# Optimization experiments

Measured on AMD Instinct MI355X. Metric: run time of the kernel, lower is better.

The kernel has to match this reference:

```python
import jax, jax.numpy as jnp
import numpy as np

N_POINTS = 131072
N_SEG = 16
C = 256
BN_EPS = 1e-5


def setup_inputs() -> dict:
    key = jax.random.key(0)
    ks = jax.random.split(key, 6)
    x = jax.random.normal(ks[0], (N_POINTS, C), jnp.float32)
    # Ragged segment end-offsets (cumulative counts), strictly increasing, last == N_POINTS.
    rng = np.random.default_rng(0)
    base = N_POINTS // N_SEG
    counts = base + rng.integers(-base // 32, base // 32, N_SEG)
    counts[-1] += N_POINTS - counts.sum()
    o = jnp.asarray(np.cumsum(counts), jnp.int32)
    s1 = 1.0 / np.sqrt(2 * C)  # linear1: Linear(2C -> C)
    s2 = 1.0 / np.sqrt(C)      # linear2: Linear(C -> C)
    W1 = jax.random.uniform(ks[1], (2 * C, C), jnp.float32, -s1, s1)
    b1 = jax.random.uniform(ks[2], (C,), jnp.float32, -s1, s1)
    W2 = jax.random.uniform(ks[3], (C, C), jnp.float32, -s2, s2)
    b2 = jax.random.uniform(ks[4], (C,), jnp.float32, -s2, s2)
    gamma = jnp.ones((C,), jnp.float32)
    beta = jnp.zeros((C,), jnp.float32)
    return {"x": x, "o": o, "W1": W1, "b1": b1, "W2": W2, "b2": b2,
            "gamma": gamma, "beta": beta}


def reference(x, o, W1, b1, W2, b2, gamma, beta):
    n, c = x.shape
    s = o.shape[0]
    # segment id per point from cumulative end-offsets
    seg_id = jnp.searchsorted(o, jnp.arange(n), side="right")  # [N]
    counts = jnp.concatenate([o[:1], o[1:] - o[:-1]])          # [S]
    # per-segment mean pooling (x_b.sum(0, True) / cnt)
    sums = jax.ops.segment_sum(x, seg_id, num_segments=s)      # [S, C]
    means = sums / counts[:, None].astype(x.dtype)
    # linear2: Linear(C, C) + ReLU on segment means
    y = jax.nn.relu(means @ W2 + b2)                           # [S, C]
    # broadcast-concat back to points, then linear1: Linear(2C, C)
    h = jnp.concatenate([x, y[seg_id]], axis=1) @ W1 + b1      # [N, C]
    # BatchNorm1d (training mode: batch statistics, biased variance) + ReLU
    mu = h.mean(axis=0)
    var = h.var(axis=0)
    out = jax.nn.relu((h - mu) * (gamma / jnp.sqrt(var + BN_EPS)) + beta)
    return out
```

## Files before the change

kernel.cpp:

```cpp
#include <hip/hip_runtime.h>
#include <stdint.h>

#define N_PTS 131072
#define NC 256
#define NSEG 16
#define BN_EPSF 1e-5f

typedef __attribute__((ext_vector_type(8))) short bf16x8;
typedef __attribute__((ext_vector_type(4))) float f32x4;

__device__ __forceinline__ unsigned short f2bf(float f) {
  union { float f; uint32_t u; } v; v.f = f;
  uint32_t u = v.u;
  uint32_t r = (u + 0x7fffu + ((u >> 16) & 1u)) >> 16;
  return (unsigned short)r;
}

__device__ __forceinline__ int swz(int col, int row) {
  return (col & ~63) | ((((col >> 3) & 7) ^ (row & 7)) << 3) | (col & 7);
}

__device__ __forceinline__ void gll16(const unsigned short* g, unsigned short* l) {
  __builtin_amdgcn_global_load_lds(
      (const __attribute__((address_space(1))) void*)g,
      (__attribute__((address_space(3))) void*)l, 16, 0, 0);
}

__global__ __launch_bounds__(256) void k_prep(const float* __restrict__ W1,
                                              unsigned short* __restrict__ w1t,
                                              float* __restrict__ zerobuf) {
  int b = blockIdx.x, t = threadIdx.x;
  if (b >= 16) {
    int i = (b - 16) * 256 + t;
    if (i < 4608) zerobuf[i] = 0.f;
    return;
  }
  __shared__ float tile[64][65];
  int bx = b & 3, by = b >> 2;
  int k0 = by * 64, j0 = bx * 64;
  int r = t >> 6, c = t & 63;
#pragma unroll
  for (int i = 0; i < 16; ++i) {
    int kk = r + i * 4;
    tile[kk][c] = W1[(size_t)(k0 + kk) * NC + j0 + c];
  }
  __syncthreads();
#pragma unroll
  for (int i = 0; i < 16; ++i) {
    int jj = r + i * 4;
    int row = j0 + jj, col = k0 + c;
    w1t[(size_t)row * NC + swz(col, row)] = f2bf(tile[c][jj]);
  }
}

__global__ __launch_bounds__(256) void k_segsum_convert(
    const float* __restrict__ x, const int* __restrict__ o,
    unsigned short* __restrict__ x_bf, float* __restrict__ seg_sums) {
  __shared__ int o_s[NSEG];
  __shared__ float s_acc[2][NC];
  int t = threadIdx.x;
  if (t < NSEG) o_s[t] = o[t];
  s_acc[0][t] = 0.f;
  s_acc[1][t] = 0.f;
  __syncthreads();
  int g = t >> 6, l = t & 63;
  int row0 = blockIdx.x * 64;
  int c0 = l * 4;
  int s0 = 0;
  while (o_s[s0] <= row0) ++s0;
  int e0 = o_s[s0];
  int s1 = (s0 < NSEG - 1) ? s0 + 1 : s0;
  float4 accA = {0.f, 0.f, 0.f, 0.f}, accB = {0.f, 0.f, 0.f, 0.f};
  const float4* xv = (const float4*)x;
#pragma unroll
  for (int i = 0; i < 16; ++i) {
    int r = row0 + g + i * 4;
    float4 v = xv[(size_t)r * 64 + l];
    ushort4 b;
    b.x = f2bf(v.x); b.y = f2bf(v.y); b.z = f2bf(v.z); b.w = f2bf(v.w);
    *(ushort4*)(x_bf + (size_t)r * NC + swz(c0, r)) = b;
    bool inA = (r < e0);
    accA.x += inA ? v.x : 0.f; accB.x += inA ? 0.f : v.x;
    accA.y += inA ? v.y : 0.f; accB.y += inA ? 0.f : v.y;
    accA.z += inA ? v.z : 0.f; accB.z += inA ? 0.f : v.z;
    accA.w += inA ? v.w : 0.f; accB.w += inA ? 0.f : v.w;
  }
  atomicAdd(&s_acc[0][c0 + 0], accA.x);
  atomicAdd(&s_acc[0][c0 + 1], accA.y);
  atomicAdd(&s_acc[0][c0 + 2], accA.z);
  atomicAdd(&s_acc[0][c0 + 3], accA.w);
  atomicAdd(&s_acc[1][c0 + 0], accB.x);
  atomicAdd(&s_acc[1][c0 + 1], accB.y);
  atomicAdd(&s_acc[1][c0 + 2], accB.z);
  atomicAdd(&s_acc[1][c0 + 3], accB.w);
  __syncthreads();
  atomicAdd(&seg_sums[s0 * NC + t], s_acc[0][t]);
  atomicAdd(&seg_sums[s1 * NC + t], s_acc[1][t]);
}

__global__ __launch_bounds__(256) void k_seg_mlp(
    const int* __restrict__ o, const float* __restrict__ seg_sums,
    const float* __restrict__ W1, const float* __restrict__ b1,
    const float* __restrict__ W2, const float* __restrict__ b2,
    float* __restrict__ z) {
  __shared__ float mean_s[NC];
  __shared__ float y_s[NC];
  int b = blockIdx.x, j = threadIdx.x;
  int start = (b == 0) ? 0 : o[b - 1];
  float inv = 1.f / (float)(o[b] - start);
  mean_s[j] = seg_sums[b * NC + j] * inv;
  __syncthreads();
  float a = b2[j];
  for (int k = 0; k < NC; ++k) a += mean_s[k] * W2[k * NC + j];
  y_s[j] = fmaxf(a, 0.f);
  __syncthreads();
  float a2 = b1[j];
  for (int k = 0; k < NC; ++k) a2 += y_s[k] * W1[(NC + k) * NC + j];
  z[b * NC + j] = a2;
}

__global__ __launch_bounds__(256) void k_gemm_stats(
    const unsigned short* __restrict__ x_bf, const unsigned short* __restrict__ w1t,
    const int* __restrict__ o, const float* __restrict__ z,
    float* __restrict__ colsum, float* __restrict__ colsumsq) {
  __shared__ __align__(16) unsigned short lA[64 * 64];
  __shared__ __align__(16) unsigned short lB[256 * 64];
  __shared__ float s_sum[NC], s_sq[NC];
  __shared__ int o_s[NSEG];
  int t = threadIdx.x, lane = t & 63, w = t >> 6;
  int row0 = blockIdx.x * 64;
  if (t < NSEG) o_s[t] = o[t];

  f32x4 acc[4][4] = {};
  for (int kt = 0; kt < 4; ++kt) {
    gll16(x_bf + (size_t)(row0 + (t >> 3)) * NC + kt * 64 + (t & 7) * 8, lA + t * 8);
    gll16(x_bf + (size_t)(row0 + (t >> 3) + 32) * NC + kt * 64 + (t & 7) * 8,
          lA + (t + 256) * 8);
#pragma unroll
    for (int i = 0; i < 8; ++i) {
      int tp = t + i * 256;
      gll16(w1t + (size_t)(tp >> 3) * NC + kt * 64 + (t & 7) * 8, lB + tp * 8);
    }
    __syncthreads();
#pragma unroll
    for (int kk = 0; kk < 2; ++kk) {
      bf16x8 af[4], bfr[4];
      int sl = kk * 4 + (lane >> 4);
#pragma unroll
      for (int mm = 0; mm < 4; ++mm) {
        int r = mm * 16 + (lane & 15);
        af[mm] = *(const bf16x8*)(lA + r * 64 + ((sl ^ (r & 7)) << 3));
      }
#pragma unroll
      for (int nn = 0; nn < 4; ++nn) {
        int jrow = w * 64 + nn * 16 + (lane & 15);
        bfr[nn] = *(const bf16x8*)(lB + jrow * 64 + ((sl ^ (jrow & 7)) << 3));
      }
#pragma unroll
      for (int mm = 0; mm < 4; ++mm)
#pragma unroll
        for (int nn = 0; nn < 4; ++nn)
          acc[mm][nn] = __builtin_amdgcn_mfma_f32_16x16x32_bf16(af[mm], bfr[nn],
                                                                acc[mm][nn], 0, 0, 0);
    }
    __syncthreads();
  }

  int s0 = 0;
  while (o_s[s0] <= row0) ++s0;
  int e0 = o_s[s0];
  int s1 = (s0 < NSEG - 1) ? s0 + 1 : s0;
  int cl = lane & 15, q = lane >> 4;
#pragma unroll
  for (int nn = 0; nn < 4; ++nn) {
    int col = w * 64 + nn * 16 + cl;
    float zA = z[s0 * NC + col], zB = z[s1 * NC + col];
    float ps = 0.f, pq = 0.f;
#pragma unroll
    for (int mm = 0; mm < 4; ++mm) {
#pragma unroll
      for (int r = 0; r < 4; ++r) {
        int row = row0 + mm * 16 + q * 4 + r;
        float hv = acc[mm][nn][r] + ((row < e0) ? zA : zB);
        ps += hv; pq += hv * hv;
      }
    }
    ps += __shfl_xor(ps, 16, 64); ps += __shfl_xor(ps, 32, 64);
    pq += __shfl_xor(pq, 16, 64); pq += __shfl_xor(pq, 32, 64);
    if (q == 0) { s_sum[col] = ps; s_sq[col] = pq; }
  }
  __syncthreads();
  atomicAdd(&colsum[t], s_sum[t]);
  atomicAdd(&colsumsq[t], s_sq[t]);
}

__global__ __launch_bounds__(256) void k_gemm_out(
    const unsigned short* __restrict__ x_bf, const unsigned short* __restrict__ w1t,
    const int* __restrict__ o, const float* __restrict__ z,
    const float* __restrict__ colsum, const float* __restrict__ colsumsq,
    const float* __restrict__ gamma, const float* __restrict__ beta,
    float* __restrict__ out) {
  __shared__ __align__(16) unsigned short lA[64 * 64];
  __shared__ __align__(16) unsigned short lB[256 * 64];
  __shared__ float s_scale[NC], s_shift[NC];
  __shared__ int o_s[NSEG];
  int t = threadIdx.x, lane = t & 63, w = t >> 6;
  int row0 = blockIdx.x * 64;
  {
    float invN = 1.f / (float)N_PTS;
    float mu = colsum[t] * invN;
    float var = colsumsq[t] * invN - mu * mu;
    float sc = gamma[t] * rsqrtf(var + BN_EPSF);
    s_scale[t] = sc;
    s_shift[t] = beta[t] - mu * sc;
  }
  if (t < NSEG) o_s[t] = o[t];

  f32x4 acc[4][4] = {};
  for (int kt = 0; kt < 4; ++kt) {
    gll16(x_bf + (size_t)(row0 + (t >> 3)) * NC + kt * 64 + (t & 7) * 8, lA + t * 8);
    gll16(x_bf + (size_t)(row0 + (t >> 3) + 32) * NC + kt * 64 + (t & 7) * 8,
          lA + (t + 256) * 8);
#pragma unroll
    for (int i = 0; i < 8; ++i) {
      int tp = t + i * 256;
      gll16(w1t + (size_t)(tp >> 3) * NC + kt * 64 + (t & 7) * 8, lB + tp * 8);
    }
    __syncthreads();
#pragma unroll
    for (int kk = 0; kk < 2; ++kk) {
      bf16x8 af[4], bfr[4];
      int sl = kk * 4 + (lane >> 4);
#pragma unroll
      for (int mm = 0; mm < 4; ++mm) {
        int r = mm * 16 + (lane & 15);
        af[mm] = *(const bf16x8*)(lA + r * 64 + ((sl ^ (r & 7)) << 3));
      }
#pragma unroll
      for (int nn = 0; nn < 4; ++nn) {
        int jrow = w * 64 + nn * 16 + (lane & 15);
        bfr[nn] = *(const bf16x8*)(lB + jrow * 64 + ((sl ^ (jrow & 7)) << 3));
      }
#pragma unroll
      for (int mm = 0; mm < 4; ++mm)
#pragma unroll
        for (int nn = 0; nn < 4; ++nn)
          acc[mm][nn] = __builtin_amdgcn_mfma_f32_16x16x32_bf16(bfr[nn], af[mm],
                                                                acc[mm][nn], 0, 0, 0);
    }
    __syncthreads();
  }

  int s0 = 0;
  while (o_s[s0] <= row0) ++s0;
  int e0 = o_s[s0];
  int s1 = (s0 < NSEG - 1) ? s0 + 1 : s0;
  int rl = lane & 15, q = lane >> 4;
#pragma unroll
  for (int mm = 0; mm < 4; ++mm) {
    int row = row0 + mm * 16 + rl;
    int sg = (row < e0) ? s0 : s1;
#pragma unroll
    for (int nn = 0; nn < 4; ++nn) {
      int c = w * 64 + nn * 16 + q * 4;
      float4 z4 = *(const float4*)(z + sg * NC + c);
      float4 sc4 = *(const float4*)(s_scale + c);
      float4 sh4 = *(const float4*)(s_shift + c);
      float4 o4;
      o4.x = fmaxf((acc[mm][nn][0] + z4.x) * sc4.x + sh4.x, 0.f);
      o4.y = fmaxf((acc[mm][nn][1] + z4.y) * sc4.y + sh4.y, 0.f);
      o4.z = fmaxf((acc[mm][nn][2] + z4.z) * sc4.z + sh4.z, 0.f);
      o4.w = fmaxf((acc[mm][nn][3] + z4.w) * sc4.w + sh4.w, 0.f);
      *(float4*)(out + (size_t)row * NC + c) = o4;
    }
  }
}

extern "C" void kernel_launch(void* const* d_in, const int* in_sizes, int n_in,
                              void* d_out, int out_size, void* d_ws, size_t ws_size,
                              hipStream_t stream) {
  const float* x = (const float*)d_in[0];
  const int* o = (const int*)d_in[1];
  const float* W1 = (const float*)d_in[2];
  const float* b1 = (const float*)d_in[3];
  const float* W2 = (const float*)d_in[4];
  const float* b2 = (const float*)d_in[5];
  const float* gamma = (const float*)d_in[6];
  const float* beta = (const float*)d_in[7];
  float* out = (float*)d_out;

  char* ws = (char*)d_ws;
  unsigned short* x_bf = (unsigned short*)ws;
  char* base2 = ws + 67108864;
  float* seg_sums = (float*)(base2);
  float* colsum   = (float*)(base2 + 16384);
  float* colsumsq = (float*)(base2 + 17408);
  float* z        = (float*)(base2 + 18432);
  unsigned short* w1t = (unsigned short*)(base2 + 34816);

  k_prep<<<34, 256, 0, stream>>>(W1, w1t, seg_sums);
  k_segsum_convert<<<2048, 256, 0, stream>>>(x, o, x_bf, seg_sums);
  k_seg_mlp<<<16, 256, 0, stream>>>(o, seg_sums, W1, b1, W2, b2, z);
  k_gemm_stats<<<2048, 256, 0, stream>>>(x_bf, w1t, o, z, colsum, colsumsq);
  k_gemm_out<<<2048, 256, 0, stream>>>(x_bf, w1t, o, z, colsum, colsumsq,
                                       gamma, beta, out);
}
```

Measured before the change: 364.9 us.

## Fuse x-side GEMM stats into convert pass; derive BN stats algebraically

The stats GEMM over x@W1[:C] now runs inside the conversion kernel, reusing the freshly converted bf16 tile kept in LDS. Per-segment column sums of g and a global sum of g^2 are accumulated there. The BatchNorm mean and variance are then rebuilt from these, the segment counts and z, using h = g + z_seg. This removes one full GEMM pass and one re-read of x_bf. In exchange LDS use per block grows (full-K A tile of 32KB plus a 32KB B tile), which may reduce occupancy, and the variance is computed in a different algebraic form.

```diff
diff --git a/kernel.cpp b/kernel.cpp
--- a/kernel.cpp
+++ b/kernel.cpp
@@ -32,7 +32,7 @@
   int b = blockIdx.x, t = threadIdx.x;
   if (b >= 16) {
     int i = (b - 16) * 256 + t;
-    if (i < 4608) zerobuf[i] = 0.f;
+    if (i < 8448) zerobuf[i] = 0.f;
     return;
   }
   __shared__ float tile[64][65];
@@ -53,49 +53,118 @@
   }
 }
 
-__global__ __launch_bounds__(256) void k_segsum_convert(
+__global__ __launch_bounds__(256) void k_gemm1(
     const float* __restrict__ x, const int* __restrict__ o,
-    unsigned short* __restrict__ x_bf, float* __restrict__ seg_sums) {
+    const unsigned short* __restrict__ w1t,
+    unsigned short* __restrict__ x_bf,
+    float* __restrict__ seg_sums, float* __restrict__ hseg,
+    float* __restrict__ gsumsq) {
+  __shared__ __align__(16) unsigned short lA[64 * NC];
+  __shared__ __align__(16) unsigned short lB[NC * 64];
+  __shared__ float s_acc[2][NC];
+  __shared__ float s_hA[NC], s_hB[NC], s_q[NC];
   __shared__ int o_s[NSEG];
-  __shared__ float s_acc[2][NC];
-  int t = threadIdx.x;
+  int t = threadIdx.x, lane = t & 63, w = t >> 6;
+  int row0 = blockIdx.x * 64;
   if (t < NSEG) o_s[t] = o[t];
   s_acc[0][t] = 0.f;
   s_acc[1][t] = 0.f;
   __syncthreads();
-  int g = t >> 6, l = t & 63;
-  int row0 = blockIdx.x * 64;
-  int c0 = l * 4;
+  int c0 = lane * 4;
   int s0 = 0;
   while (o_s[s0] <= row0) ++s0;
   int e0 = o_s[s0];
   int s1 = (s0 < NSEG - 1) ? s0 + 1 : s0;
-  float4 accA = {0.f, 0.f, 0.f, 0.f}, accB = {0.f, 0.f, 0.f, 0.f};
-  const float4* xv = (const float4*)x;
-#pragma unroll
-  for (int i = 0; i < 16; ++i) {
-    int r = row0 + g + i * 4;
-    float4 v = xv[(size_t)r * 64 + l];
-    ushort4 b;
-    b.x = f2bf(v.x); b.y = f2bf(v.y); b.z = f2bf(v.z); b.w = f2bf(v.w);
-    *(ushort4*)(x_bf + (size_t)r * NC + swz(c0, r)) = b;
-    bool inA = (r < e0);
-    accA.x += inA ? v.x : 0.f; accB.x += inA ? 0.f : v.x;
-    accA.y += inA ? v.y : 0.f; accB.y += inA ? 0.f : v.y;
-    accA.z += inA ? v.z : 0.f; accB.z += inA ? 0.f : v.z;
-    accA.w += inA ? v.w : 0.f; accB.w += inA ? 0.f : v.w;
-  }
-  atomicAdd(&s_acc[0][c0 + 0], accA.x);
-  atomicAdd(&s_acc[0][c0 + 1], accA.y);
-  atomicAdd(&s_acc[0][c0 + 2], accA.z);
-  atomicAdd(&s_acc[0][c0 + 3], accA.w);
-  atomicAdd(&s_acc[1][c0 + 0], accB.x);
-  atomicAdd(&s_acc[1][c0 + 1], accB.y);
-  atomicAdd(&s_acc[1][c0 + 2], accB.z);
-  atomicAdd(&s_acc[1][c0 + 3], accB.w);
+
+  {
+    float4 accA = {0.f, 0.f, 0.f, 0.f}, accB = {0.f, 0.f, 0.f, 0.f};
+    const float4* xv = (const float4*)x;
+#pragma unroll
+    for (int i = 0; i < 16; ++i) {
+      int rl = w + i * 4;
+      int r = row0 + rl;
+      float4 v = xv[(size_t)r * 64 + lane];
+      ushort4 b;
+      b.x = f2bf(v.x); b.y = f2bf(v.y); b.z = f2bf(v.z); b.w = f2bf(v.w);
+      int sc = swz(c0, r);
+      *(ushort4*)(x_bf + (size_t)r * NC + sc) = b;
+      *(ushort4*)(lA + rl * NC + sc) = b;
+      bool inA = (r < e0);
+      accA.x += inA ? v.x : 0.f; accB.x += inA ? 0.f : v.x;
+      accA.y += inA ? v.y : 0.f; accB.y += inA ? 0.f : v.y;
+      accA.z += inA ? v.z : 0.f; accB.z += inA ? 0.f : v.z;
+      accA.w += inA ? v.w : 0.f; accB.w += inA ? 0.f : v.w;
+    }
+    atomicAdd(&s_acc[0][c0 + 0], accA.x);
+    atomicAdd(&s_acc[0][c0 + 1], accA.y);
+    atomicAdd(&s_acc[0][c0 + 2], accA.z);
+    atomicAdd(&s_acc[0][c0 + 3], accA.w);
+    atomicAdd(&s_acc[1][c0 + 0], accB.x);
+    atomicAdd(&s_acc[1][c0 + 1], accB.y);
+    atomicAdd(&s_acc[1][c0 + 2], accB.z);
+    atomicAdd(&s_acc[1][c0 + 3], accB.w);
+  }
+
+  f32x4 acc[4][4] = {};
+  for (int kt = 0; kt < 4; ++kt) {
+#pragma unroll
+    for (int i = 0; i < 8; ++i) {
+      int tp = t + i * 256;
+      gll16(w1t + (size_t)(tp >> 3) * NC + kt * 64 + (t & 7) * 8, lB + tp * 8);
+    }
+    __syncthreads();
+#pragma unroll
+    for (int kk = 0; kk < 2; ++kk) {
+      bf16x8 af[4], bfr[4];
+      int sl = kk * 4 + (lane >> 4);
+#pragma unroll
+      for (int mm = 0; mm < 4; ++mm) {
+        int r = mm * 16 + (lane & 15);
+        af[mm] = *(const bf16x8*)(lA + r * NC + kt * 64 + ((sl ^ (r & 7)) << 3));
+      }
+#pragma unroll
+      for (int nn = 0; nn < 4; ++nn) {
+        int jrow = w * 64 + nn * 16 + (lane & 15);
+        bfr[nn] = *(const bf16x8*)(lB + jrow * 64 + ((sl ^ (jrow & 7)) << 3));
+      }
+#pragma unroll
+      for (int mm = 0; mm < 4; ++mm)
+#pragma unroll
+        for (int nn = 0; nn < 4; ++nn)
+          acc[mm][nn] = __builtin_amdgcn_mfma_f32_16x16x32_bf16(af[mm], bfr[nn],
+                                                                acc[mm][nn], 0, 0, 0);
+    }
+    __syncthreads();
+  }
+
+  int cl = lane & 15, q = lane >> 4;
+#pragma unroll
+  for (int nn = 0; nn < 4; ++nn) {
+    int col = w * 64 + nn * 16 + cl;
+    float pA = 0.f, pB = 0.f, pq = 0.f;
+#pragma unroll
+    for (int mm = 0; mm < 4; ++mm) {
+#pragma unroll
+      for (int r_ = 0; r_ < 4; ++r_) {
+        int row = row0 + mm * 16 + q * 4 + r_;
+        float gv = acc[mm][nn][r_];
+        bool inA = (row < e0);
+        pA += inA ? gv : 0.f;
+        pB += inA ? 0.f : gv;
+        pq += gv * gv;
+      }
+    }
+    pA += __shfl_xor(pA, 16, 64); pA += __shfl_xor(pA, 32, 64);
+    pB += __shfl_xor(pB, 16, 64); pB += __shfl_xor(pB, 32, 64);
+    pq += __shfl_xor(pq, 16, 64); pq += __shfl_xor(pq, 32, 64);
+    if (q == 0) { s_hA[col] = pA; s_hB[col] = pB; s_q[col] = pq; }
+  }
   __syncthreads();
   atomicAdd(&seg_sums[s0 * NC + t], s_acc[0][t]);
   atomicAdd(&seg_sums[s1 * NC + t], s_acc[1][t]);
+  atomicAdd(&hseg[s0 * NC + t], s_hA[t]);
+  atomicAdd(&hseg[s1 * NC + t], s_hB[t]);
+  atomicAdd(&gsumsq[t], s_q[t]);
 }
 
 __global__ __launch_bounds__(256) void k_seg_mlp(
@@ -119,23 +188,45 @@
   z[b * NC + j] = a2;
 }
 
-__global__ __launch_bounds__(256) void k_gemm_stats(
+__global__ __launch_bounds__(256) void k_gemm2(
     const unsigned short* __restrict__ x_bf, const unsigned short* __restrict__ w1t,
     const int* __restrict__ o, const float* __restrict__ z,
-    float* __restrict__ colsum, float* __restrict__ colsumsq) {
-  __shared__ __align__(16) unsigned short lA[64 * 64];
-  __shared__ __align__(16) unsigned short lB[256 * 64];
-  __shared__ float s_sum[NC], s_sq[NC];
+    const float* __restrict__ hseg, const float* __restrict__ gsumsq,
+    const float* __restrict__ gamma, const float* __restrict__ beta,
+    float* __restrict__ out) {
+  __shared__ __align__(16) unsigned short lA[64 * NC];
+  __shared__ __align__(16) unsigned short lB[NC * 64];
+  __shared__ float s_scale[NC], s_shift[NC];
   __shared__ int o_s[NSEG];
   int t = threadIdx.x, lane = t & 63, w = t >> 6;
   int row0 = blockIdx.x * 64;
   if (t < NSEG) o_s[t] = o[t];
-
+  __syncthreads();
+  {
+    float cs = 0.f, cq = gsumsq[t];
+    int prev = 0;
+#pragma unroll
+    for (int s = 0; s < NSEG; ++s) {
+      float cnt = (float)(o_s[s] - prev);
+      prev = o_s[s];
+      float hs = hseg[s * NC + t], zz = z[s * NC + t];
+      cs += hs + cnt * zz;
+      cq += (2.f * hs + cnt * zz) * zz;
+    }
+    float invN = 1.f / (float)N_PTS;
+    float mu = cs * invN;
+    float var = cq * invN - mu * mu;
+    float sc = gamma[t] * rsqrtf(var + BN_EPSF);
+    s_scale[t] = sc;
+    s_shift[t] = beta[t] - mu * sc;
+  }
+#pragma unroll
+  for (int i = 0; i < 8; ++i) {
+    int tp = t + i * 256;
+    gll16(x_bf + (size_t)(row0 + (tp >> 5)) * NC + (tp & 31) * 8, lA + tp * 8);
+  }
   f32x4 acc[4][4] = {};
   for (int kt = 0; kt < 4; ++kt) {
-    gll16(x_bf + (size_t)(row0 + (t >> 3)) * NC + kt * 64 + (t & 7) * 8, lA + t * 8);
-    gll16(x_bf + (size_t)(row0 + (t >> 3) + 32) * NC + kt * 64 + (t & 7) * 8,
-          lA + (t + 256) * 8);
 #pragma unroll
     for (int i = 0; i < 8; ++i) {
       int tp = t + i * 256;
@@ -149,7 +240,7 @@
 #pragma unroll
       for (int mm = 0; mm < 4; ++mm) {
         int r = mm * 16 + (lane & 15);
-        af[mm] = *(const bf16x8*)(lA + r * 64 + ((sl ^ (r & 7)) << 3));
+        af[mm] = *(const bf16x8*)(lA + r * NC + kt * 64 + ((sl ^ (r & 7)) << 3));
       }
 #pragma unroll
       for (int nn = 0; nn < 4; ++nn) {
@@ -160,97 +251,11 @@
       for (int mm = 0; mm < 4; ++mm)
 #pragma unroll
         for (int nn = 0; nn < 4; ++nn)
-          acc[mm][nn] = __builtin_amdgcn_mfma_f32_16x16x32_bf16(af[mm], bfr[nn],
-                                                                acc[mm][nn], 0, 0, 0);
-    }
-    __syncthreads();
-  }
-
-  int s0 = 0;
-  while (o_s[s0] <= row0) ++s0;
-  int e0 = o_s[s0];
-  int s1 = (s0 < NSEG - 1) ? s0 + 1 : s0;
-  int cl = lane & 15, q = lane >> 4;
-#pragma unroll
-  for (int nn = 0; nn < 4; ++nn) {
-    int col = w * 64 + nn * 16 + cl;
-    float zA = z[s0 * NC + col], zB = z[s1 * NC + col];
-    float ps = 0.f, pq = 0.f;
-#pragma unroll
-    for (int mm = 0; mm < 4; ++mm) {
-#pragma unroll
-      for (int r = 0; r < 4; ++r) {
-        int row = row0 + mm * 16 + q * 4 + r;
-        float hv = acc[mm][nn][r] + ((row < e0) ? zA : zB);
-        ps += hv; pq += hv * hv;
-      }
-    }
-    ps += __shfl_xor(ps, 16, 64); ps += __shfl_xor(ps, 32, 64);
-    pq += __shfl_xor(pq, 16, 64); pq += __shfl_xor(pq, 32, 64);
-    if (q == 0) { s_sum[col] = ps; s_sq[col] = pq; }
-  }
-  __syncthreads();
-  atomicAdd(&colsum[t], s_sum[t]);
-  atomicAdd(&colsumsq[t], s_sq[t]);
-}
-
-__global__ __launch_bounds__(256) void k_gemm_out(
-    const unsigned short* __restrict__ x_bf, const unsigned short* __restrict__ w1t,
-    const int* __restrict__ o, const float* __restrict__ z,
-    const float* __restrict__ colsum, const float* __restrict__ colsumsq,
-    const float* __restrict__ gamma, const float* __restrict__ beta,
-    float* __restrict__ out) {
-  __shared__ __align__(16) unsigned short lA[64 * 64];
-  __shared__ __align__(16) unsigned short lB[256 * 64];
-  __shared__ float s_scale[NC], s_shift[NC];
-  __shared__ int o_s[NSEG];
-  int t = threadIdx.x, lane = t & 63, w = t >> 6;
-  int row0 = blockIdx.x * 64;
-  {
-    float invN = 1.f / (float)N_PTS;
-    float mu = colsum[t] * invN;
-    float var = colsumsq[t] * invN - mu * mu;
-    float sc = gamma[t] * rsqrtf(var + BN_EPSF);
-    s_scale[t] = sc;
-    s_shift[t] = beta[t] - mu * sc;
-  }
-  if (t < NSEG) o_s[t] = o[t];
-
-  f32x4 acc[4][4] = {};
-  for (int kt = 0; kt < 4; ++kt) {
-    gll16(x_bf + (size_t)(row0 + (t >> 3)) * NC + kt * 64 + (t & 7) * 8, lA + t * 8);
-    gll16(x_bf + (size_t)(row0 + (t >> 3) + 32) * NC + kt * 64 + (t & 7) * 8,
-          lA + (t + 256) * 8);
-#pragma unroll
-    for (int i = 0; i < 8; ++i) {
-      int tp = t + i * 256;
-      gll16(w1t + (size_t)(tp >> 3) * NC + kt * 64 + (t & 7) * 8, lB + tp * 8);
-    }
-    __syncthreads();
-#pragma unroll
-    for (int kk = 0; kk < 2; ++kk) {
-      bf16x8 af[4], bfr[4];
-      int sl = kk * 4 + (lane >> 4);
-#pragma unroll
-      for (int mm = 0; mm < 4; ++mm) {
-        int r = mm * 16 + (lane & 15);
-        af[mm] = *(const bf16x8*)(lA + r * 64 + ((sl ^ (r & 7)) << 3));
-      }
-#pragma unroll
-      for (int nn = 0; nn < 4; ++nn) {
-        int jrow = w * 64 + nn * 16 + (lane & 15);
-        bfr[nn] = *(const bf16x8*)(lB + jrow * 64 + ((sl ^ (jrow & 7)) << 3));
-      }
-#pragma unroll
-      for (int mm = 0; mm < 4; ++mm)
-#pragma unroll
-        for (int nn = 0; nn < 4; ++nn)
           acc[mm][nn] = __builtin_amdgcn_mfma_f32_16x16x32_bf16(bfr[nn], af[mm],
                                                                 acc[mm][nn], 0, 0, 0);
     }
     __syncthreads();
   }
-
   int s0 = 0;
   while (o_s[s0] <= row0) ++s0;
   int e0 = o_s[s0];
@@ -293,15 +298,14 @@
   unsigned short* x_bf = (unsigned short*)ws;
   char* base2 = ws + 67108864;
   float* seg_sums = (float*)(base2);
-  float* colsum   = (float*)(base2 + 16384);
-  float* colsumsq = (float*)(base2 + 17408);
-  float* z        = (float*)(base2 + 18432);
-  unsigned short* w1t = (unsigned short*)(base2 + 34816);
-
-  k_prep<<<34, 256, 0, stream>>>(W1, w1t, seg_sums);
-  k_segsum_convert<<<2048, 256, 0, stream>>>(x, o, x_bf, seg_sums);
+  float* hseg     = (float*)(base2 + 16384);
+  float* gsumsq   = (float*)(base2 + 32768);
+  float* z        = (float*)(base2 + 33792);
+  unsigned short* w1t = (unsigned short*)(base2 + 50176);
+
+  k_prep<<<49, 256, 0, stream>>>(W1, w1t, seg_sums);
+  k_gemm1<<<2048, 256, 0, stream>>>(x, o, w1t, x_bf, seg_sums, hseg, gsumsq);
   k_seg_mlp<<<16, 256, 0, stream>>>(o, seg_sums, W1, b1, W2, b2, z);
-  k_gemm_stats<<<2048, 256, 0, stream>>>(x_bf, w1t, o, z, colsum, colsumsq);
-  k_gemm_out<<<2048, 256, 0, stream>>>(x_bf, w1t, o, z, colsum, colsumsq,
-                                       gamma, beta, out);
-}
+  k_gemm2<<<2048, 256, 0, stream>>>(x_bf, w1t, o, z, hseg, gsumsq,
+                                    gamma, beta, out);
+}
```

After: 346.5 us. 5.0% less time.
